# Optimization experiments

Hardware: AMD Instinct MI355X
Metric: run time of the kernel (lower is better)

Reference implementation:

```python
import jax, jax.numpy as jnp
import numpy as np

B, T, C = 4, 2048, 2048
H, N = 32, 64          # num_heads, head_size
EPS = 1e-5 * 8.0 ** 2  # GroupNorm eps = 1e-5 * head_size_divisor**2


def setup_inputs() -> dict:
    key = jax.random.key(0)
    ks = jax.random.split(key, 20)
    f = lambda i, shape, s=0.02: jax.random.normal(ks[i], shape, jnp.float32) * s
    return {
        'hidden': jax.random.normal(ks[0], (B, T, C), jnp.float32),
        'time_maa_x': f(1, (C,)), 'time_maa_w': f(2, (C,)), 'time_maa_k': f(3, (C,)),
        'time_maa_v': f(4, (C,)), 'time_maa_r': f(5, (C,)), 'time_maa_g': f(6, (C,)),
        'time_maa_w1': f(7, (C, 160)), 'time_maa_w2': f(8, (5, 32, C)),
        'time_decay': f(9, (C,), 0.5), 'time_decay_w1': f(10, (C, 64)),
        'time_decay_w2': f(11, (64, C)),
        'time_faaaa': f(12, (H, N), 0.5),
        'w_r': f(13, (C, C)), 'w_k': f(14, (C, C)), 'w_v': f(15, (C, C)),
        'w_g': f(16, (C, C)), 'w_o': f(17, (C, C)),
        'ln_w': jnp.ones((C,), jnp.float32), 'ln_b': jnp.zeros((C,), jnp.float32),
    }


def reference(hidden, time_maa_x, time_maa_w, time_maa_k, time_maa_v, time_maa_r,
              time_maa_g, time_maa_w1, time_maa_w2, time_decay, time_decay_w1,
              time_decay_w2, time_faaaa, w_r, w_k, w_v, w_g, w_o, ln_w, ln_b):
    x = hidden
    # time_shift: prepend zero row, drop last (state=None path)
    shifted = jnp.pad(x, ((0, 0), (1, 0), (0, 0)))[:, :-1]
    xx = shifted - x
    # data-dependent low-rank token-shift interpolation (5 lerp channels)
    xm = x + xx * time_maa_x
    t5 = jnp.tanh(jnp.einsum('btc,ce->bte', xm, time_maa_w1)).reshape(B, T, 5, 32)
    m = jnp.einsum('btfe,fec->fbtc', t5, time_maa_w2)  # [5,B,T,C]
    mw, mk, mv, mr, mg = m[0], m[1], m[2], m[3], m[4]
    xd = x + xx * (time_maa_w + mw)
    xk = x + xx * (time_maa_k + mk)
    xv = x + xx * (time_maa_v + mv)
    xr = x + xx * (time_maa_r + mr)
    xg = x + xx * (time_maa_g + mg)
    r = xr @ w_r.T
    k = xk @ w_k.T
    v = xv @ w_v.T
    g = jax.nn.silu(xg @ w_g.T)
    td = time_decay + jnp.tanh(xd @ time_decay_w1) @ time_decay_w2  # [B,T,C]
    w = jnp.exp(-jnp.exp(td))  # per-channel decay in (0,1)
    # [B,T,C] -> [T,B,H,N] for the scan
    to_tbhn = lambda a: a.reshape(B, T, H, N).transpose(1, 0, 2, 3)
    rT, kT, vT, wT = to_tbhn(r), to_tbhn(k), to_tbhn(v), to_tbhn(w)
    u = time_faaaa  # [H,N]
    state0 = jnp.zeros((B, H, N, N), jnp.float32)  # [B,H,key,value]

    def step(state, ins):
        r_t, k_t, v_t, w_t = ins  # each [B,H,N]
        att = k_t[..., :, None] * v_t[..., None, :]        # outer product k v^T
        out_t = jnp.einsum('bhn,bhnm->bhm', r_t,
                           u[None, :, :, None] * att + state)
        new_state = att + w_t[..., None] * state           # decay along key dim
        return new_state, out_t

    _, outs = jax.lax.scan(step, state0, (rT, kT, vT, wT))  # outs [T,B,H,N]
    out = outs.transpose(1, 0, 2, 3)                         # [B,T,H,N]
    # GroupNorm with H groups over C channels, applied per (b,t) sample
    mu = out.mean(-1, keepdims=True)
    var = out.var(-1, keepdims=True)
    out = (out - mu) / jnp.sqrt(var + EPS)
    out = (out * ln_w.reshape(H, N) + ln_b.reshape(H, N)).reshape(B, T, C)
    out = out * g
    return out @ w_o.T
```

## Files before the change

kernel.cpp:

```cpp
#include <hip/hip_runtime.h>
#include <hip/hip_bf16.h>
#include <math.h>

typedef __hip_bfloat16 bf16;
typedef __attribute__((ext_vector_type(8))) short short8;
typedef __attribute__((ext_vector_type(4))) float f32x4;

#define Bb 4
#define Tt 2048
#define Cc 2048
#define Hh 32
#define Nn 64
#define BT (Bb*Tt)
#define Gg 16
#define Ll 128
#define SPLITK 8

__device__ __forceinline__ float b2f(bf16 x) { return __bfloat162float(x); }
__device__ __forceinline__ bf16  f2b(float x) { return __float2bfloat16(x); }

__global__ __launch_bounds__(256) void cvt_kernel(
    const float* __restrict__ in, bf16* __restrict__ out)
{
  int i = blockIdx.x * 256 + threadIdx.x;
  out[i] = f2b(in[i]);
}

__global__ __launch_bounds__(256) void cvt_t2_kernel(
    const float* __restrict__ in, bf16* __restrict__ hi, bf16* __restrict__ lo,
    int N)
{
  int idx = blockIdx.x * 256 + threadIdx.x;
  int n = idx >> 11, k = idx & 2047;
  float v = in[(size_t)k * N + n];
  bf16 h = f2b(v);
  hi[idx] = h;
  lo[idx] = f2b(v - b2f(h));
}

__global__ __launch_bounds__(256) void cvt_w2t_kernel(
    const float* __restrict__ in, bf16* __restrict__ hi, bf16* __restrict__ lo)
{
  int idx = blockIdx.x * 256 + threadIdx.x;
  int c = idx / 160, e = idx - c * 160;
  float v = in[(size_t)e * Cc + c];
  bf16 h = f2b(v);
  hi[idx] = h;
  lo[idx] = f2b(v - b2f(h));
}

__global__ __launch_bounds__(256) void prep_xm_kernel(
    const float* __restrict__ x, const float* __restrict__ maa_x,
    bf16* __restrict__ xm)
{
  int idx = blockIdx.x * 256 + threadIdx.x;
  int c  = idx & (Cc - 1);
  int bt = idx >> 11;
  int t  = bt & (Tt - 1);
  float xv   = x[idx];
  float prev = (t == 0) ? 0.f : x[idx - Cc];
  xm[idx] = f2b(xv + (prev - xv) * maa_x[c]);
}

#define LDA 40

__global__ __launch_bounds__(256) void mfma_gemm_kernel(
    const bf16* __restrict__ A, const bf16* __restrict__ B,
    bf16* __restrict__ outB, float* __restrict__ outF, int mode)
{
  __shared__ bf16 As[128 * LDA];
  __shared__ bf16 Bs[128 * LDA];
  int tid  = threadIdx.x;
  int lane = tid & 63, wid = tid >> 6;
  int wm = wid & 1, wn = wid >> 1;
  int quad = lane >> 4, l16 = lane & 15;
  size_t rowBase = (size_t)blockIdx.x * 128;
  size_t colBase = (size_t)blockIdx.y * 128;

  f32x4 acc[4][4];
  #pragma unroll
  for (int i = 0; i < 4; ++i)
    #pragma unroll
    for (int j = 0; j < 4; ++j)
      acc[i][j] = (f32x4){0.f, 0.f, 0.f, 0.f};

  for (int k0 = 0; k0 < 2048; k0 += 32) {
    #pragma unroll
    for (int pass = 0; pass < 2; ++pass) {
      int chunk = tid + pass * 256;
      int row = chunk >> 2, kc = (chunk & 3) * 8;
      short8 av = *(const short8*)(A + (rowBase + row) * 2048 + k0 + kc);
      short8 bv = *(const short8*)(B + (colBase + row) * 2048 + k0 + kc);
      *(short8*)(As + row * LDA + kc) = av;
      *(short8*)(Bs + row * LDA + kc) = bv;
    }
    __syncthreads();
    short8 af[4], bf[4];
    #pragma unroll
    for (int i = 0; i < 4; ++i) {
      af[i] = *(const short8*)(As + (wm * 64 + i * 16 + l16) * LDA + quad * 8);
      bf[i] = *(const short8*)(Bs + (wn * 64 + i * 16 + l16) * LDA + quad * 8);
    }
    #pragma unroll
    for (int i = 0; i < 4; ++i)
      #pragma unroll
      for (int j = 0; j < 4; ++j)
        acc[i][j] = __builtin_amdgcn_mfma_f32_16x16x32_bf16(af[i], bf[j], acc[i][j], 0, 0, 0);
    __syncthreads();
  }

  #pragma unroll
  for (int i = 0; i < 4; ++i) {
    #pragma unroll
    for (int j = 0; j < 4; ++j) {
      int gc = colBase + wn * 64 + j * 16 + l16;
      #pragma unroll
      for (int reg = 0; reg < 4; ++reg) {
        int gr = rowBase + wm * 64 + i * 16 + quad * 4 + reg;
        float v = acc[i][j][reg];
        size_t idx = (size_t)gr * 2048 + gc;
        if (mode == 0)      outB[idx] = f2b(v);
        else if (mode == 2) outB[idx] = f2b(v / (1.f + expf(-v)));
        else                outF[idx] = v;
      }
    }
  }
}

template<int NF>
__global__ __launch_bounds__(256) void mfma_skinny_kernel(
    const bf16* __restrict__ A, const bf16* __restrict__ Bt_hi,
    const bf16* __restrict__ Bt_lo,
    float* __restrict__ partial, int kseg_len)
{
  constexpr int N = NF * 16;
  __shared__ bf16 As[64 * LDA];
  __shared__ bf16 Bs[2 * N * LDA];
  int tid = threadIdx.x;
  int lane = tid & 63, w = tid >> 6;
  int quad = lane >> 4, l16 = lane & 15;
  int rowBase = blockIdx.x * 64;
  int kbeg = blockIdx.y * kseg_len;

  f32x4 acc[NF];
  #pragma unroll
  for (int f = 0; f < NF; ++f) acc[f] = (f32x4){0.f, 0.f, 0.f, 0.f};

  for (int k0 = kbeg; k0 < kbeg + kseg_len; k0 += 32) {
    {
      int row = tid >> 2, kc = (tid & 3) * 8;
      *(short8*)(As + row * LDA + kc) =
          *(const short8*)(A + (size_t)(rowBase + row) * 2048 + k0 + kc);
    }
    for (int c = tid; c < N * 8; c += 256) {
      int half = c >= N * 4;
      int cc = c - half * N * 4;
      int row = cc >> 2, kc = (cc & 3) * 8;
      const bf16* src = half ? Bt_lo : Bt_hi;
      *(short8*)(Bs + (half * N + row) * LDA + kc) =
          *(const short8*)(src + (size_t)row * 2048 + k0 + kc);
    }
    __syncthreads();
    short8 af = *(const short8*)(As + (w * 16 + l16) * LDA + quad * 8);
    #pragma unroll
    for (int f = 0; f < NF; ++f) {
      short8 bh = *(const short8*)(Bs + (f * 16 + l16) * LDA + quad * 8);
      short8 bl = *(const short8*)(Bs + ((N + f * 16 + l16)) * LDA + quad * 8);
      acc[f] = __builtin_amdgcn_mfma_f32_16x16x32_bf16(af, bh, acc[f], 0, 0, 0);
      acc[f] = __builtin_amdgcn_mfma_f32_16x16x32_bf16(af, bl, acc[f], 0, 0, 0);
    }
    __syncthreads();
  }

  #pragma unroll
  for (int f = 0; f < NF; ++f) {
    int gc = f * 16 + l16;
    #pragma unroll
    for (int reg = 0; reg < 4; ++reg) {
      int gr = rowBase + w * 16 + quad * 4 + reg;
      partial[((size_t)blockIdx.y * 8192 + gr) * N + gc] = acc[f][reg];
    }
  }
}

__global__ __launch_bounds__(256) void reduce_tanh_kernel(
    const float* __restrict__ partial, bf16* __restrict__ out, int MN)
{
  int idx = blockIdx.x * 256 + threadIdx.x;
  float s = 0.f;
  #pragma unroll
  for (int j = 0; j < SPLITK; ++j) s += partial[(size_t)j * MN + idx];
  out[idx] = f2b(tanhf(s));
}

#define BM 128
#define BN 128
#define BKk 16

__global__ __launch_bounds__(256) void gemm_kernel(
    const bf16* __restrict__ A, const float* __restrict__ Bm,
    bf16* __restrict__ outB,
    const float* __restrict__ bias,
    int M, int N, int K, int transB, int mode)
{
  __shared__ float As[BKk][BM + 1];
  __shared__ float Bs[BKk][BN + 1];
  int tid = threadIdx.x;
  int rowBase = blockIdx.x * BM;
  int colBase = blockIdx.y * BN;
  int tx = tid & 15, ty = tid >> 4;
  float acc[8][8];
  #pragma unroll
  for (int i = 0; i < 8; ++i)
    #pragma unroll
    for (int j = 0; j < 8; ++j) acc[i][j] = 0.f;

  for (int k0 = 0; k0 < K; k0 += BKk) {
    #pragma unroll
    for (int i = 0; i < 8; ++i) {
      int lin = tid + i * 256;
      int r = lin >> 4, kk = lin & 15;
      int gr = rowBase + r, gk = k0 + kk;
      float val = 0.f;
      if (gr < M && gk < K) val = b2f(A[(size_t)gr * K + gk]);
      As[kk][r] = val;
    }
    #pragma unroll
    for (int i = 0; i < 8; ++i) {
      int lin = tid + i * 256;
      float val = 0.f;
      if (transB) {
        int n = lin >> 4, kk = lin & 15;
        int gn = colBase + n, gk = k0 + kk;
        if (gn < N && gk < K) val = Bm[(size_t)gn * K + gk];
        Bs[kk][n] = val;
      } else {
        int kk = lin >> 7, n = lin & 127;
        int gn = colBase + n, gk = k0 + kk;
        if (gn < N && gk < K) val = Bm[(size_t)gk * N + gn];
        Bs[kk][n] = val;
      }
    }
    __syncthreads();
    #pragma unroll
    for (int kk = 0; kk < BKk; ++kk) {
      float a[8], b[8];
      #pragma unroll
      for (int i = 0; i < 8; ++i) a[i] = As[kk][ty * 8 + i];
      #pragma unroll
      for (int j = 0; j < 8; ++j) b[j] = Bs[kk][tx * 8 + j];
      #pragma unroll
      for (int i = 0; i < 8; ++i)
        #pragma unroll
        for (int j = 0; j < 8; ++j)
          acc[i][j] = fmaf(a[i], b[j], acc[i][j]);
    }
    __syncthreads();
  }
  #pragma unroll
  for (int i = 0; i < 8; ++i) {
    int gr = rowBase + ty * 8 + i;
    if (gr >= M) continue;
    #pragma unroll
    for (int j = 0; j < 8; ++j) {
      int gn = colBase + tx * 8 + j;
      if (gn >= N) continue;
      float v = acc[i][j];
      size_t idx = (size_t)gr * N + gn;
      if (mode == 1)      outB[idx] = f2b(tanhf(v));
      else                outB[idx] = f2b(bias[gn] + v);
    }
  }
}

__global__ __launch_bounds__(256) void lerp5_mfma_kernel(
    const float* __restrict__ x, const bf16* __restrict__ t5,
    const bf16* __restrict__ w2t_hi, const bf16* __restrict__ w2t_lo,
    const float* __restrict__ maa_w, const float* __restrict__ maa_k,
    const float* __restrict__ maa_v, const float* __restrict__ maa_r,
    const float* __restrict__ maa_g,
    bf16* __restrict__ xd, bf16* __restrict__ xk, bf16* __restrict__ xv_,
    bf16* __restrict__ xr, bf16* __restrict__ xg)
{
  int tid  = threadIdx.x;
  int lane = tid & 63, wid = tid >> 6;
  int wm = wid & 1, wn = wid >> 1;
  int quad = lane >> 4, l16 = lane & 15;
  int rowBase = blockIdx.x * 128;
  int colBase = blockIdx.y * 128;

  const float* maas[5] = {maa_w, maa_k, maa_v, maa_r, maa_g};
  bf16* outs[5] = {xd, xk, xv_, xr, xg};

  #pragma unroll
  for (int f = 0; f < 5; ++f) {
    short8 af[4];
    #pragma unroll
    for (int i = 0; i < 4; ++i)
      af[i] = *(const short8*)(t5 +
          (size_t)(rowBase + wm * 64 + i * 16 + l16) * 160 + f * 32 + quad * 8);

    f32x4 acc[4][4];
    #pragma unroll
    for (int i = 0; i < 4; ++i)
      #pragma unroll
      for (int j = 0; j < 4; ++j)
        acc[i][j] = (f32x4){0.f, 0.f, 0.f, 0.f};

    #pragma unroll
    for (int j = 0; j < 4; ++j) {
      size_t boff = (size_t)(colBase + wn * 64 + j * 16 + l16) * 160 + f * 32 + quad * 8;
      short8 bh = *(const short8*)(w2t_hi + boff);
      short8 bl = *(const short8*)(w2t_lo + boff);
      #pragma unroll
      for (int i = 0; i < 4; ++i) {
        acc[i][j] = __builtin_amdgcn_mfma_f32_16x16x32_bf16(af[i], bh, acc[i][j], 0, 0, 0);
        acc[i][j] = __builtin_amdgcn_mfma_f32_16x16x32_bf16(af[i], bl, acc[i][j], 0, 0, 0);
      }
    }

    const float* maa = maas[f];
    bf16* outp = outs[f];
    #pragma unroll
    for (int j = 0; j < 4; ++j) {
      int gc = colBase + wn * 64 + j * 16 + l16;
      float mv = maa[gc];
      #pragma unroll
      for (int i = 0; i < 4; ++i) {
        #pragma unroll
        for (int reg = 0; reg < 4; ++reg) {
          int gr = rowBase + wm * 64 + i * 16 + quad * 4 + reg;
          size_t idx = (size_t)gr * Cc + gc;
          float xv0  = x[idx];
          float prev = ((gr & (Tt - 1)) == 0) ? 0.f : x[idx - Cc];
          outp[idx] = f2b(xv0 + (prev - xv0) * (mv + acc[i][j][reg]));
        }
      }
    }
  }
}

__global__ __launch_bounds__(256) void wkv_local_kernel(
    const bf16* __restrict__ k, const bf16* __restrict__ v,
    const bf16* __restrict__ td,
    float* __restrict__ S_local, float* __restrict__ wp)
{
  int bh = blockIdx.x >> 4;
  int c  = blockIdx.x & 15;
  int b  = bh >> 5, h = bh & 31;
  int tid = threadIdx.x;
  int m = tid & 63, chunk = tid >> 6;
  __shared__ float kw[2][64][2];
  __shared__ float vsb[2][64];
  float s[16], wpr[16];
  #pragma unroll
  for (int i = 0; i < 16; ++i) { s[i] = 0.f; wpr[i] = 1.f; }
  size_t base = (size_t)b * Tt * Cc + (size_t)(c * Ll) * Cc + (size_t)h * 64;
  for (int t = 0; t < Ll; ++t, base += Cc) {
    int p = t & 1;
    int role = tid >> 6, ch = tid & 63;
    if (role == 0)      kw[p][ch][0] = b2f(k[base + ch]);
    else if (role == 1) kw[p][ch][1] = expf(-expf(b2f(td[base + ch])));
    else if (role == 2) vsb[p][ch]   = b2f(v[base + ch]);
    __syncthreads();
    float vm = vsb[p][m];
    #pragma unroll
    for (int i = 0; i < 16; ++i) {
      float kk = kw[p][chunk * 16 + i][0];
      float ww = kw[p][chunk * 16 + i][1];
      s[i] = fmaf(ww, s[i], kk * vm);
      wpr[i] *= ww;
    }
  }
  size_t sb = ((size_t)blockIdx.x * 64 + chunk * 16) * 64 + m;
  #pragma unroll
  for (int i = 0; i < 16; ++i) S_local[sb + (size_t)i * 64] = s[i];
  if (m == 0) {
    int wb = blockIdx.x * 64 + chunk * 16;
    #pragma unroll
    for (int i = 0; i < 16; ++i) wp[wb + i] = wpr[i];
  }
}

__global__ __launch_bounds__(256) void wkv_combine_kernel(
    const float* __restrict__ S_local, const float* __restrict__ wp,
    float* __restrict__ S_start)
{
  int idx = blockIdx.x * 256 + threadIdx.x;
  int m = idx & 63;
  int n = (idx >> 6) & 63;
  int bh = idx >> 12;
  float cur = 0.f;
  #pragma unroll
  for (int c = 0; c < Gg; ++c) {
    size_t sbase = (((size_t)(bh * Gg + c)) * 64 + n) * 64 + m;
    S_start[sbase] = cur;
    cur = fmaf(wp[(bh * Gg + c) * 64 + n], cur, S_local[sbase]);
  }
}

__global__ __launch_bounds__(256) void wkv_out_kernel(
    const bf16* __restrict__ r, const bf16* __restrict__ k,
    const bf16* __restrict__ v, const bf16* __restrict__ td,
    const float* __restrict__ u, const float* __restrict__ S_start,
    bf16* __restrict__ out)
{
  int bh = blockIdx.x >> 4;
  int c  = blockIdx.x & 15;
  int b  = bh >> 5, h = bh & 31;
  int tid = threadIdx.x;
  int m = tid & 63, chunk = tid >> 6;
  __shared__ float4 rkw[64];
  __shared__ float vsb[64];
  __shared__ float red[256];
  float s[16], ureg[16];
  size_t sb = ((size_t)blockIdx.x * 64 + chunk * 16) * 64 + m;
  #pragma unroll
  for (int i = 0; i < 16; ++i) {
    s[i]    = S_start[sb + (size_t)i * 64];
    ureg[i] = u[h * 64 + chunk * 16 + i];
  }
  size_t base = (size_t)b * Tt * Cc + (size_t)(c * Ll) * Cc + (size_t)h * 64;
  for (int t = 0; t < Ll; ++t, base += Cc) {
    int role = tid >> 6, ch = tid & 63;
    if (role == 0)      rkw[ch].x = b2f(r[base + ch]);
    else if (role == 1) rkw[ch].y = b2f(k[base + ch]);
    else if (role == 2) rkw[ch].z = expf(-expf(b2f(td[base + ch])));
    else                vsb[ch]   = b2f(v[base + ch]);
    __syncthreads();
    float vm = vsb[m];
    float acc = 0.f;
    #pragma unroll
    for (int i = 0; i < 16; ++i) {
      float4 q = rkw[chunk * 16 + i];
      float kv = q.y * vm;
      acc = fmaf(q.x, fmaf(ureg[i], kv, s[i]), acc);
      s[i] = fmaf(q.z, s[i], kv);
    }
    red[tid] = acc;
    __syncthreads();
    if (tid < 64)
      out[base + tid] = f2b(red[tid] + red[tid + 64] + red[tid + 128] + red[tid + 192]);
  }
}

__global__ __launch_bounds__(256) void gn_gate_kernel(
    const bf16* __restrict__ wkv, const bf16* __restrict__ g,
    const float* __restrict__ lnw, const float* __restrict__ lnb,
    bf16* __restrict__ out)
{
  int bt = blockIdx.x;
  int wv = threadIdx.x >> 6, lane = threadIdx.x & 63;
  const float EPS = 6.4e-4f;
  for (int h = wv; h < Hh; h += 4) {
    size_t base = (size_t)bt * Cc + h * 64;
    float x = b2f(wkv[base + lane]);
    float s = x, s2 = x * x;
    #pragma unroll
    for (int off = 1; off < 64; off <<= 1) {
      s  += __shfl_xor(s, off);
      s2 += __shfl_xor(s2, off);
    }
    float mean = s * (1.f / 64.f);
    float var  = s2 * (1.f / 64.f) - mean * mean;
    float inv  = rsqrtf(var + EPS);
    float normed = (x - mean) * inv * lnw[h * 64 + lane] + lnb[h * 64 + lane];
    out[base + lane] = f2b(normed * b2f(g[base + lane]));
  }
}

extern "C" void kernel_launch(void* const* d_in, const int* in_sizes, int n_in,
                              void* d_out, int out_size, void* d_ws, size_t ws_size,
                              hipStream_t stream) {
  const float* hidden = (const float*)d_in[0];
  const float* maa_x  = (const float*)d_in[1];
  const float* maa_w  = (const float*)d_in[2];
  const float* maa_k  = (const float*)d_in[3];
  const float* maa_v  = (const float*)d_in[4];
  const float* maa_r  = (const float*)d_in[5];
  const float* maa_g  = (const float*)d_in[6];
  const float* maa_w1 = (const float*)d_in[7];
  const float* maa_w2 = (const float*)d_in[8];
  const float* tdecay = (const float*)d_in[9];
  const float* dw1    = (const float*)d_in[10];
  const float* dw2    = (const float*)d_in[11];
  const float* faaaa  = (const float*)d_in[12];
  const float* w_r    = (const float*)d_in[13];
  const float* w_k    = (const float*)d_in[14];
  const float* w_v    = (const float*)d_in[15];
  const float* w_g    = (const float*)d_in[16];
  const float* w_o    = (const float*)d_in[17];
  const float* lnw    = (const float*)d_in[18];
  const float* lnb    = (const float*)d_in[19];
  float* outF = (float*)d_out;
  bf16* rscratch = (bf16*)d_out;

  char* ws = (char*)d_ws;
  const size_t BUF  = (size_t)BT * Cc * sizeof(bf16);
  const size_t WBUF = (size_t)Cc * Cc * sizeof(bf16);
  const size_t MB = 1024 * 1024;
  bf16* buf0 = (bf16*)(ws + 0 * BUF);
  bf16* buf1 = (bf16*)(ws + 1 * BUF);
  bf16* buf2 = (bf16*)(ws + 2 * BUF);
  bf16* buf3 = (bf16*)(ws + 3 * BUF);
  bf16* buf4 = (bf16*)(ws + 4 * BUF);
  char* small = ws + 5 * BUF;
  bf16* t5buf   = (bf16*)(small + 0);
  bf16* abuf    = (bf16*)(small + 4 * MB);
  bf16* w1t_hi  = (bf16*)(small + 5 * MB);
  bf16* w1t_lo  = (bf16*)(small + 5 * MB + 768 * 1024);
  bf16* dw1t_hi = (bf16*)(small + 6 * MB + 512 * 1024);
  bf16* dw1t_lo = (bf16*)(small + 6 * MB + 768 * 1024);
  char* wbase = small + 8 * MB;
  bf16* wrb = (bf16*)(wbase + 0 * WBUF);
  bf16* wkb = (bf16*)(wbase + 1 * WBUF);
  bf16* wvb = (bf16*)(wbase + 2 * WBUF);
  bf16* wgb = (bf16*)(wbase + 3 * WBUF);
  bf16* wob = (bf16*)(wbase + 4 * WBUF);

  bf16* w2t_hi = (bf16*)((char*)d_out + 48 * MB);
  bf16* w2t_lo = (bf16*)((char*)d_out + 49 * MB);

  float* slbuf = (float*)((char*)d_out + BUF);
  float* ssbuf = (float*)buf0;
  float* wpbuf = (float*)t5buf;
  float* pbuf  = (float*)d_out;

  dim3 blk(256);
  const int CVT_G = Cc * Cc / 256;

  cvt_kernel<<<dim3(CVT_G), blk, 0, stream>>>(w_r, wrb);
  cvt_kernel<<<dim3(CVT_G), blk, 0, stream>>>(w_k, wkb);
  cvt_kernel<<<dim3(CVT_G), blk, 0, stream>>>(w_v, wvb);
  cvt_kernel<<<dim3(CVT_G), blk, 0, stream>>>(w_g, wgb);
  cvt_kernel<<<dim3(CVT_G), blk, 0, stream>>>(w_o, wob);
  cvt_t2_kernel<<<dim3(160 * Cc / 256), blk, 0, stream>>>(maa_w1, w1t_hi, w1t_lo, 160);
  cvt_t2_kernel<<<dim3(64 * Cc / 256), blk, 0, stream>>>(dw1, dw1t_hi, dw1t_lo, 64);
  cvt_w2t_kernel<<<dim3(160 * Cc / 256), blk, 0, stream>>>(maa_w2, w2t_hi, w2t_lo);

  prep_xm_kernel<<<dim3(BT * Cc / 256), blk, 0, stream>>>(hidden, maa_x, buf0);

  mfma_skinny_kernel<10><<<dim3(128, SPLITK), blk, 0, stream>>>(
      buf0, w1t_hi, w1t_lo, pbuf, 2048 / SPLITK);
  reduce_tanh_kernel<<<dim3(BT * 160 / 256), blk, 0, stream>>>(pbuf, t5buf,
                                                               BT * 160);

  lerp5_mfma_kernel<<<dim3(64, 16), blk, 0, stream>>>(hidden, t5buf,
      w2t_hi, w2t_lo, maa_w, maa_k, maa_v, maa_r, maa_g,
      buf1, buf2, buf3, buf4, buf0);

  mfma_skinny_kernel<4><<<dim3(128, SPLITK), blk, 0, stream>>>(
      buf1, dw1t_hi, dw1t_lo, pbuf, 2048 / SPLITK);
  reduce_tanh_kernel<<<dim3(BT * 64 / 256), blk, 0, stream>>>(pbuf, abuf,
                                                              BT * 64);
  gemm_kernel<<<dim3(64, 16), blk, 0, stream>>>(abuf, dw2, buf1, tdecay,
                                                BT, Cc, 64, 0, 3);

  mfma_gemm_kernel<<<dim3(64, 16), blk, 0, stream>>>(buf4, wrb, rscratch, nullptr, 0);
  mfma_gemm_kernel<<<dim3(64, 16), blk, 0, stream>>>(buf2, wkb, buf4, nullptr, 0);
  mfma_gemm_kernel<<<dim3(64, 16), blk, 0, stream>>>(buf3, wvb, buf2, nullptr, 0);
  mfma_gemm_kernel<<<dim3(64, 16), blk, 0, stream>>>(buf0, wgb, buf3, nullptr, 2);

  wkv_local_kernel<<<dim3(Bb * Hh * Gg), blk, 0, stream>>>(buf4, buf2, buf1,
                                                           slbuf, wpbuf);
  wkv_combine_kernel<<<dim3(Bb * Hh * Nn * Nn / 256), blk, 0, stream>>>(
      slbuf, wpbuf, ssbuf);
  wkv_out_kernel<<<dim3(Bb * Hh * Gg), blk, 0, stream>>>(rscratch, buf4, buf2,
      buf1, faaaa, ssbuf, buf1);

  gn_gate_kernel<<<dim3(BT), blk, 0, stream>>>(buf1, buf3, lnw, lnb, buf4);

  mfma_gemm_kernel<<<dim3(64, 16), blk, 0, stream>>>(buf4, wob, nullptr, outF, 4);
}
```

Measured before the change: 1.830 ms.

## Use direct global-to-LDS loads in GEMM and double-buffer WKV output step

The main GEMM now stages tiles with global_load_lds straight into unpadded shared memory, so tile data no longer passes through registers. Separately, the WKV output kernel double-buffers its shared scratch and defers each step's reduction and store to the next iteration, cutting one barrier per timestep. The unpadded layout can cause LDS bank conflicts on fragment reads, and correctness depends on the async LDS loads being complete when __syncthreads runs.

Result: slower. 1.933 ms (+5.6%).

```diff
diff --git a/kernel.cpp b/kernel.cpp
--- a/kernel.cpp
+++ b/kernel.cpp
@@ -19,6 +19,12 @@
 __device__ __forceinline__ float b2f(bf16 x) { return __bfloat162float(x); }
 __device__ __forceinline__ bf16  f2b(float x) { return __float2bfloat16(x); }
 
+__device__ __forceinline__ void gload16(const bf16* g, bf16* l) {
+  __builtin_amdgcn_global_load_lds(
+      (const __attribute__((address_space(1))) void*)g,
+      (__attribute__((address_space(3))) void*)l, 16, 0, 0);
+}
+
 __global__ __launch_bounds__(256) void cvt_kernel(
     const float* __restrict__ in, bf16* __restrict__ out)
 {
@@ -62,14 +68,12 @@
   xm[idx] = f2b(xv + (prev - xv) * maa_x[c]);
 }
 
-#define LDA 40
-
 __global__ __launch_bounds__(256) void mfma_gemm_kernel(
     const bf16* __restrict__ A, const bf16* __restrict__ B,
     bf16* __restrict__ outB, float* __restrict__ outF, int mode)
 {
-  __shared__ bf16 As[128 * LDA];
-  __shared__ bf16 Bs[128 * LDA];
+  __shared__ bf16 As[128 * 32];
+  __shared__ bf16 Bs[128 * 32];
   int tid  = threadIdx.x;
   int lane = tid & 63, wid = tid >> 6;
   int wm = wid & 1, wn = wid >> 1;
@@ -77,6 +81,13 @@
   size_t rowBase = (size_t)blockIdx.x * 128;
   size_t colBase = (size_t)blockIdx.y * 128;
 
+  int seg0 = wid * 2, seg1 = seg0 + 1;
+  int scol = (lane & 3) * 8;
+  const bf16* ga0 = A + (rowBase + seg0 * 16 + (lane >> 2)) * 2048 + scol;
+  const bf16* ga1 = A + (rowBase + seg1 * 16 + (lane >> 2)) * 2048 + scol;
+  const bf16* gb0 = B + (colBase + seg0 * 16 + (lane >> 2)) * 2048 + scol;
+  const bf16* gb1 = B + (colBase + seg1 * 16 + (lane >> 2)) * 2048 + scol;
+
   f32x4 acc[4][4];
   #pragma unroll
   for (int i = 0; i < 4; ++i)
@@ -85,21 +96,16 @@
       acc[i][j] = (f32x4){0.f, 0.f, 0.f, 0.f};
 
   for (int k0 = 0; k0 < 2048; k0 += 32) {
-    #pragma unroll
-    for (int pass = 0; pass < 2; ++pass) {
-      int chunk = tid + pass * 256;
-      int row = chunk >> 2, kc = (chunk & 3) * 8;
-      short8 av = *(const short8*)(A + (rowBase + row) * 2048 + k0 + kc);
-      short8 bv = *(const short8*)(B + (colBase + row) * 2048 + k0 + kc);
-      *(short8*)(As + row * LDA + kc) = av;
-      *(short8*)(Bs + row * LDA + kc) = bv;
-    }
+    gload16(ga0 + k0, As + seg0 * 512);
+    gload16(ga1 + k0, As + seg1 * 512);
+    gload16(gb0 + k0, Bs + seg0 * 512);
+    gload16(gb1 + k0, Bs + seg1 * 512);
     __syncthreads();
     short8 af[4], bf[4];
     #pragma unroll
     for (int i = 0; i < 4; ++i) {
-      af[i] = *(const short8*)(As + (wm * 64 + i * 16 + l16) * LDA + quad * 8);
-      bf[i] = *(const short8*)(Bs + (wn * 64 + i * 16 + l16) * LDA + quad * 8);
+      af[i] = *(const short8*)(As + (wm * 64 + i * 16 + l16) * 32 + quad * 8);
+      bf[i] = *(const short8*)(Bs + (wn * 64 + i * 16 + l16) * 32 + quad * 8);
     }
     #pragma unroll
     for (int i = 0; i < 4; ++i)
@@ -126,6 +132,8 @@
     }
   }
 }
+
+#define LDA 40
 
 template<int NF>
 __global__ __launch_bounds__(256) void mfma_skinny_kernel(
@@ -410,9 +418,9 @@
   int b  = bh >> 5, h = bh & 31;
   int tid = threadIdx.x;
   int m = tid & 63, chunk = tid >> 6;
-  __shared__ float4 rkw[64];
-  __shared__ float vsb[64];
-  __shared__ float red[256];
+  __shared__ float4 rkw[2][64];
+  __shared__ float vsb[2][64];
+  __shared__ float red[2][256];
   float s[16], ureg[16];
   size_t sb = ((size_t)blockIdx.x * 64 + chunk * 16) * 64 + m;
   #pragma unroll
@@ -422,26 +430,34 @@
   }
   size_t base = (size_t)b * Tt * Cc + (size_t)(c * Ll) * Cc + (size_t)h * 64;
   for (int t = 0; t < Ll; ++t, base += Cc) {
+    int p = t & 1;
     int role = tid >> 6, ch = tid & 63;
-    if (role == 0)      rkw[ch].x = b2f(r[base + ch]);
-    else if (role == 1) rkw[ch].y = b2f(k[base + ch]);
-    else if (role == 2) rkw[ch].z = expf(-expf(b2f(td[base + ch])));
-    else                vsb[ch]   = b2f(v[base + ch]);
-    __syncthreads();
-    float vm = vsb[m];
+    if (role == 0)      rkw[p][ch].x = b2f(r[base + ch]);
+    else if (role == 1) rkw[p][ch].y = b2f(k[base + ch]);
+    else if (role == 2) rkw[p][ch].z = expf(-expf(b2f(td[base + ch])));
+    else                vsb[p][ch]   = b2f(v[base + ch]);
+    __syncthreads();
+    if (t > 0 && tid < 64) {
+      int q = p ^ 1;
+      out[base - Cc + tid] =
+          f2b(red[q][tid] + red[q][tid + 64] + red[q][tid + 128] + red[q][tid + 192]);
+    }
+    float vm = vsb[p][m];
     float acc = 0.f;
     #pragma unroll
     for (int i = 0; i < 16; ++i) {
-      float4 q = rkw[chunk * 16 + i];
-      float kv = q.y * vm;
-      acc = fmaf(q.x, fmaf(ureg[i], kv, s[i]), acc);
-      s[i] = fmaf(q.z, s[i], kv);
-    }
-    red[tid] = acc;
-    __syncthreads();
-    if (tid < 64)
-      out[base + tid] = f2b(red[tid] + red[tid + 64] + red[tid + 128] + red[tid + 192]);
-  }
+      float4 q4 = rkw[p][chunk * 16 + i];
+      float kv = q4.y * vm;
+      acc = fmaf(q4.x, fmaf(ureg[i], kv, s[i]), acc);
+      s[i] = fmaf(q4.z, s[i], kv);
+    }
+    red[p][tid] = acc;
+  }
+  __syncthreads();
+  int q = (Ll - 1) & 1;
+  if (tid < 64)
+    out[base - Cc + tid] =
+        f2b(red[q][tid] + red[q][tid + 64] + red[q][tid + 128] + red[q][tid + 192]);
 }
 
 __global__ __launch_bounds__(256) void gn_gate_kernel(
```

## Run WKV scan kernels as single wavefronts with register-blocked state and prefetch

Applied to the files above, without the earlier changes.

Both chunked WKV kernels (local state and output) now run with 64 threads per block instead of 256. Each lane holds a 16x4 tile of the per-head state and reads k/w/v/r from double-buffered shared memory with vector loads. Because the block is a single wavefront, the per-timestep __syncthreads barriers become lgkmcnt waits, and the next timestep's inputs are loaded from global memory before the current step is computed. This removes barrier and LDS traffic from the serial time loop. In exchange there are fewer wavefronts per CU to hide latency, and each lane needs more registers.

Measured after the change: 1.765 ms. 1.04x faster.

```diff
diff --git a/kernel.cpp b/kernel.cpp
--- a/kernel.cpp
+++ b/kernel.cpp
@@ -340,7 +340,7 @@
   }
 }
 
-__global__ __launch_bounds__(256) void wkv_local_kernel(
+__global__ __launch_bounds__(64) void wkv_local_kernel(
     const bf16* __restrict__ k, const bf16* __restrict__ v,
     const bf16* __restrict__ td,
     float* __restrict__ S_local, float* __restrict__ wp)
@@ -348,37 +348,52 @@
   int bh = blockIdx.x >> 4;
   int c  = blockIdx.x & 15;
   int b  = bh >> 5, h = bh & 31;
-  int tid = threadIdx.x;
-  int m = tid & 63, chunk = tid >> 6;
-  __shared__ float kw[2][64][2];
-  __shared__ float vsb[2][64];
-  float s[16], wpr[16];
-  #pragma unroll
-  for (int i = 0; i < 16; ++i) { s[i] = 0.f; wpr[i] = 1.f; }
+  int j  = threadIdx.x;
+  int cn = j >> 4, mg = j & 15;
+  __shared__ __align__(16) float kb[2][64];
+  __shared__ __align__(16) float wb[2][64];
+  __shared__ __align__(16) float vb[2][64];
+  f32x4 s[16];
+  float wpr[16];
+  #pragma unroll
+  for (int i = 0; i < 16; ++i) { s[i] = (f32x4){0.f,0.f,0.f,0.f}; wpr[i] = 1.f; }
+
   size_t base = (size_t)b * Tt * Cc + (size_t)(c * Ll) * Cc + (size_t)h * 64;
+  float kv_ = b2f(k[base + j]);
+  float wv_ = expf(-expf(b2f(td[base + j])));
+  float vv_ = b2f(v[base + j]);
   for (int t = 0; t < Ll; ++t, base += Cc) {
     int p = t & 1;
-    int role = tid >> 6, ch = tid & 63;
-    if (role == 0)      kw[p][ch][0] = b2f(k[base + ch]);
-    else if (role == 1) kw[p][ch][1] = expf(-expf(b2f(td[base + ch])));
-    else if (role == 2) vsb[p][ch]   = b2f(v[base + ch]);
-    __syncthreads();
-    float vm = vsb[p][m];
-    #pragma unroll
-    for (int i = 0; i < 16; ++i) {
-      float kk = kw[p][chunk * 16 + i][0];
-      float ww = kw[p][chunk * 16 + i][1];
-      s[i] = fmaf(ww, s[i], kk * vm);
-      wpr[i] *= ww;
-    }
-  }
-  size_t sb = ((size_t)blockIdx.x * 64 + chunk * 16) * 64 + m;
-  #pragma unroll
-  for (int i = 0; i < 16; ++i) S_local[sb + (size_t)i * 64] = s[i];
-  if (m == 0) {
-    int wb = blockIdx.x * 64 + chunk * 16;
-    #pragma unroll
-    for (int i = 0; i < 16; ++i) wp[wb + i] = wpr[i];
+    kb[p][j] = kv_; wb[p][j] = wv_; vb[p][j] = vv_;
+    size_t nb = base + ((t + 1 < Ll) ? Cc : 0);
+    kv_ = b2f(k[nb + j]);
+    wv_ = expf(-expf(b2f(td[nb + j])));
+    vv_ = b2f(v[nb + j]);
+    asm volatile("s_waitcnt lgkmcnt(0)" ::: "memory");
+    f32x4 vm = *(const f32x4*)(&vb[p][mg * 4]);
+    #pragma unroll
+    for (int i4 = 0; i4 < 4; ++i4) {
+      f32x4 k4 = *(const f32x4*)(&kb[p][cn * 16 + i4 * 4]);
+      f32x4 w4 = *(const f32x4*)(&wb[p][cn * 16 + i4 * 4]);
+      #pragma unroll
+      for (int q = 0; q < 4; ++q) {
+        int i = i4 * 4 + q;
+        float kn = k4[q], wn = w4[q];
+        s[i].x = fmaf(wn, s[i].x, kn * vm.x);
+        s[i].y = fmaf(wn, s[i].y, kn * vm.y);
+        s[i].z = fmaf(wn, s[i].z, kn * vm.z);
+        s[i].w = fmaf(wn, s[i].w, kn * vm.w);
+        wpr[i] *= wn;
+      }
+    }
+  }
+  #pragma unroll
+  for (int i = 0; i < 16; ++i)
+    *(f32x4*)(&S_local[((size_t)blockIdx.x * 64 + cn * 16 + i) * 64 + mg * 4]) = s[i];
+  if (mg == 0) {
+    #pragma unroll
+    for (int i = 0; i < 16; ++i)
+      wp[blockIdx.x * 64 + cn * 16 + i] = wpr[i];
   }
 }
 
@@ -399,7 +414,7 @@
   }
 }
 
-__global__ __launch_bounds__(256) void wkv_out_kernel(
+__global__ __launch_bounds__(64) void wkv_out_kernel(
     const bf16* __restrict__ r, const bf16* __restrict__ k,
     const bf16* __restrict__ v, const bf16* __restrict__ td,
     const float* __restrict__ u, const float* __restrict__ S_start,
@@ -408,39 +423,61 @@
   int bh = blockIdx.x >> 4;
   int c  = blockIdx.x & 15;
   int b  = bh >> 5, h = bh & 31;
-  int tid = threadIdx.x;
-  int m = tid & 63, chunk = tid >> 6;
-  __shared__ float4 rkw[64];
-  __shared__ float vsb[64];
-  __shared__ float red[256];
-  float s[16], ureg[16];
-  size_t sb = ((size_t)blockIdx.x * 64 + chunk * 16) * 64 + m;
+  int j  = threadIdx.x;
+  int cn = j >> 4, mg = j & 15;
+  __shared__ __align__(16) float rb[2][64];
+  __shared__ __align__(16) float kb[2][64];
+  __shared__ __align__(16) float wb[2][64];
+  __shared__ __align__(16) float vb[2][64];
+  __shared__ __align__(16) float red[256];
+  f32x4 s[16];
+  float ur[16];
   #pragma unroll
   for (int i = 0; i < 16; ++i) {
-    s[i]    = S_start[sb + (size_t)i * 64];
-    ureg[i] = u[h * 64 + chunk * 16 + i];
-  }
+    s[i]  = *(const f32x4*)(&S_start[((size_t)blockIdx.x * 64 + cn * 16 + i) * 64 + mg * 4]);
+    ur[i] = u[h * 64 + cn * 16 + i];
+  }
+
   size_t base = (size_t)b * Tt * Cc + (size_t)(c * Ll) * Cc + (size_t)h * 64;
+  float rv_ = b2f(r[base + j]);
+  float kv_ = b2f(k[base + j]);
+  float wv_ = expf(-expf(b2f(td[base + j])));
+  float vv_ = b2f(v[base + j]);
   for (int t = 0; t < Ll; ++t, base += Cc) {
-    int role = tid >> 6, ch = tid & 63;
-    if (role == 0)      rkw[ch].x = b2f(r[base + ch]);
-    else if (role == 1) rkw[ch].y = b2f(k[base + ch]);
-    else if (role == 2) rkw[ch].z = expf(-expf(b2f(td[base + ch])));
-    else                vsb[ch]   = b2f(v[base + ch]);
-    __syncthreads();
-    float vm = vsb[m];
-    float acc = 0.f;
-    #pragma unroll
-    for (int i = 0; i < 16; ++i) {
-      float4 q = rkw[chunk * 16 + i];
-      float kv = q.y * vm;
-      acc = fmaf(q.x, fmaf(ureg[i], kv, s[i]), acc);
-      s[i] = fmaf(q.z, s[i], kv);
-    }
-    red[tid] = acc;
-    __syncthreads();
-    if (tid < 64)
-      out[base + tid] = f2b(red[tid] + red[tid + 64] + red[tid + 128] + red[tid + 192]);
+    int p = t & 1;
+    rb[p][j] = rv_; kb[p][j] = kv_; wb[p][j] = wv_; vb[p][j] = vv_;
+    size_t nb = base + ((t + 1 < Ll) ? Cc : 0);
+    rv_ = b2f(r[nb + j]);
+    kv_ = b2f(k[nb + j]);
+    wv_ = expf(-expf(b2f(td[nb + j])));
+    vv_ = b2f(v[nb + j]);
+    asm volatile("s_waitcnt lgkmcnt(0)" ::: "memory");
+    f32x4 vm = *(const f32x4*)(&vb[p][mg * 4]);
+    f32x4 acc = (f32x4){0.f, 0.f, 0.f, 0.f};
+    #pragma unroll
+    for (int i4 = 0; i4 < 4; ++i4) {
+      f32x4 r4 = *(const f32x4*)(&rb[p][cn * 16 + i4 * 4]);
+      f32x4 k4 = *(const f32x4*)(&kb[p][cn * 16 + i4 * 4]);
+      f32x4 w4 = *(const f32x4*)(&wb[p][cn * 16 + i4 * 4]);
+      #pragma unroll
+      for (int q = 0; q < 4; ++q) {
+        int i = i4 * 4 + q;
+        float rn = r4[q], kn = k4[q], wn = w4[q], un = ur[i];
+        float kvx = kn * vm.x, kvy = kn * vm.y, kvz = kn * vm.z, kvw = kn * vm.w;
+        acc.x = fmaf(rn, fmaf(un, kvx, s[i].x), acc.x);
+        acc.y = fmaf(rn, fmaf(un, kvy, s[i].y), acc.y);
+        acc.z = fmaf(rn, fmaf(un, kvz, s[i].z), acc.z);
+        acc.w = fmaf(rn, fmaf(un, kvw, s[i].w), acc.w);
+        s[i].x = fmaf(wn, s[i].x, kvx);
+        s[i].y = fmaf(wn, s[i].y, kvy);
+        s[i].z = fmaf(wn, s[i].z, kvz);
+        s[i].w = fmaf(wn, s[i].w, kvw);
+      }
+    }
+    *(f32x4*)(&red[4 * j]) = acc;
+    asm volatile("s_waitcnt lgkmcnt(0)" ::: "memory");
+    float o = red[j] + red[64 + j] + red[128 + j] + red[192 + j];
+    out[base + j] = f2b(o);
   }
 }
 
@@ -561,12 +598,12 @@
   mfma_gemm_kernel<<<dim3(64, 16), blk, 0, stream>>>(buf3, wvb, buf2, nullptr, 0);
   mfma_gemm_kernel<<<dim3(64, 16), blk, 0, stream>>>(buf0, wgb, buf3, nullptr, 2);
 
-  wkv_local_kernel<<<dim3(Bb * Hh * Gg), blk, 0, stream>>>(buf4, buf2, buf1,
-                                                           slbuf, wpbuf);
+  wkv_local_kernel<<<dim3(Bb * Hh * Gg), dim3(64), 0, stream>>>(
+      buf4, buf2, buf1, slbuf, wpbuf);
   wkv_combine_kernel<<<dim3(Bb * Hh * Nn * Nn / 256), blk, 0, stream>>>(
       slbuf, wpbuf, ssbuf);
-  wkv_out_kernel<<<dim3(Bb * Hh * Gg), blk, 0, stream>>>(rscratch, buf4, buf2,
-      buf1, faaaa, ssbuf, buf1);
+  wkv_out_kernel<<<dim3(Bb * Hh * Gg), dim3(64), 0, stream>>>(
+      rscratch, buf4, buf2, buf1, faaaa, ssbuf, buf1);
 
   gn_gate_kernel<<<dim3(BT), blk, 0, stream>>>(buf1, buf3, lnw, lnb, buf4);
 
```
